# Optimization experiments

Measured on AMD Instinct MI355X. Metric: run time of the kernel, lower is better.

Reference implementation:

```python
import jax, jax.numpy as jnp
import numpy as np

N_NODES = 100000
N_EDGES = 600000
D_FEAT = 128
N_CLASSES = 64


def setup_inputs() -> dict:
    key = jax.random.key(0)
    k_h, k_src, k_dst, k_w = jax.random.split(key, 4)
    h = jax.random.normal(k_h, (N_NODES, D_FEAT), dtype=jnp.float32)
    src = jax.random.randint(k_src, (N_EDGES,), 0, N_NODES, dtype=jnp.int64)
    dst = jax.random.randint(k_dst, (N_EDGES,), 0, N_NODES, dtype=jnp.int64)
    # nn.Linear(2*D_FEAT, N_CLASSES): weight [out, in], bias [out]
    W = jax.random.normal(k_w, (N_CLASSES, 2 * D_FEAT), dtype=jnp.float32) * (1.0 / np.sqrt(2 * D_FEAT))
    b = jnp.zeros((N_CLASSES,), dtype=jnp.float32)
    return {"h": h, "src": src, "dst": dst, "W": W, "b": b}


def reference(h, src, dst, W, b):
    # score = Linear(concat([h[src], h[dst]], -1))
    # Split W to avoid materializing the [n_edges, 2*d] concat:
    # concat @ W.T == h[src] @ W[:, :d].T + h[dst] @ W[:, d:].T
    d = h.shape[1]
    Wu = W[:, :d]  # [out, d]
    Wv = W[:, d:]  # [out, d]
    score = (jnp.einsum('ed,cd->ec', h[src], Wu)
             + jnp.einsum('ed,cd->ec', h[dst], Wv)
             + b)
    return score  # [n_edges, out_classes]
```

## Files before the change

kernel.cpp:

```cpp
#include <hip/hip_runtime.h>

#define N_NODES   100000
#define N_EDGES   600000
#define D_FEAT    128
#define N_CLASSES 64

typedef short bf16x8 __attribute__((ext_vector_type(8)));
typedef float f32x4  __attribute__((ext_vector_type(4)));
typedef unsigned short u16x8 __attribute__((ext_vector_type(8)));

__device__ __forceinline__ unsigned short f2bf(float f) {
    unsigned int u = __float_as_uint(f);
    unsigned int r = (u + 0x7fffu + ((u >> 16) & 1u)) >> 16;
    return (unsigned short)r;
}
__device__ __forceinline__ float bf2f(unsigned short u) {
    return __uint_as_float((unsigned int)u << 16);
}

__global__ __launch_bounds__(256) void build_wcat(const float* __restrict__ W,
                                                  unsigned short* __restrict__ Wc) {
    int idx = blockIdx.x * 256 + threadIdx.x;
    int c = idx >> 7;
    int k = idx & 127;
    float v = (c < 64) ? W[c * 256 + k] : W[(c - 64) * 256 + 128 + k];
    Wc[c * 128 + k] = f2bf(v);
}

__global__ __launch_bounds__(256) void proj_mfma(const float* __restrict__ h,
                                                 const unsigned short* __restrict__ Wc,
                                                 const float* __restrict__ b,
                                                 unsigned short* __restrict__ P) {
    const int wave = (blockIdx.x * 256 + threadIdx.x) >> 6;
    const int lane = threadIdx.x & 63;
    const int n0   = wave * 16;
    if (n0 >= N_NODES) return;
    const int m    = lane & 15;
    const int quad = lane >> 4;

    bf16x8 hfrag[4];
    const float* hrow = h + (size_t)(n0 + m) * 128 + quad * 8;
#pragma unroll
    for (int ks = 0; ks < 4; ++ks) {
        f32x4 v0 = __builtin_nontemporal_load((const f32x4*)(hrow + ks * 32));
        f32x4 v1 = __builtin_nontemporal_load((const f32x4*)(hrow + ks * 32 + 4));
        bf16x8 a;
        a[0] = (short)f2bf(v0[0]); a[1] = (short)f2bf(v0[1]);
        a[2] = (short)f2bf(v0[2]); a[3] = (short)f2bf(v0[3]);
        a[4] = (short)f2bf(v1[0]); a[5] = (short)f2bf(v1[1]);
        a[6] = (short)f2bf(v1[2]); a[7] = (short)f2bf(v1[3]);
        hfrag[ks] = a;
    }

    f32x4 acc[8];
#pragma unroll
    for (int ct = 0; ct < 8; ++ct) acc[ct] = (f32x4){0.f, 0.f, 0.f, 0.f};

#pragma unroll
    for (int ct = 0; ct < 8; ++ct) {
        const unsigned short* wrow = Wc + (size_t)(ct * 16 + m) * 128 + quad * 8;
#pragma unroll
        for (int ks = 0; ks < 4; ++ks) {
            bf16x8 wfrag = *(const bf16x8*)(wrow + ks * 32);
            acc[ct] = __builtin_amdgcn_mfma_f32_16x16x32_bf16(wfrag, hfrag[ks], acc[ct], 0, 0, 0);
        }
    }

    const int node = n0 + m;
    unsigned short* prow = P + (size_t)node * 128;
#pragma unroll
    for (int ct = 0; ct < 8; ++ct) {
        const int cb = ct * 16 + quad * 4;
        float v[4];
        if (cb < 64) {
            f32x4 bb = *(const f32x4*)(b + cb);
#pragma unroll
            for (int r = 0; r < 4; ++r) v[r] = acc[ct][r] + bb[r];
        } else {
#pragma unroll
            for (int r = 0; r < 4; ++r) v[r] = acc[ct][r];
        }
        ushort4 pk;
        pk.x = f2bf(v[0]); pk.y = f2bf(v[1]);
        pk.z = f2bf(v[2]); pk.w = f2bf(v[3]);
        *(ushort4*)(prow + cb) = pk;
    }
}

__global__ __launch_bounds__(256) void edge_kernel(const int* __restrict__ src,
                                                   const int* __restrict__ dst,
                                                   const unsigned short* __restrict__ P,
                                                   float* __restrict__ out) {
    int g  = blockIdx.x * 256 + threadIdx.x;
    int e  = g >> 3;
    int c0 = (g & 7) << 3;
    int s = src[e];
    int d = dst[e];
    u16x8 us = *(const u16x8*)(P + (size_t)s * 128 + c0);
    u16x8 ud = *(const u16x8*)(P + (size_t)d * 128 + 64 + c0);
    f32x4 o0, o1;
    o0[0] = bf2f(us[0]) + bf2f(ud[0]);
    o0[1] = bf2f(us[1]) + bf2f(ud[1]);
    o0[2] = bf2f(us[2]) + bf2f(ud[2]);
    o0[3] = bf2f(us[3]) + bf2f(ud[3]);
    o1[0] = bf2f(us[4]) + bf2f(ud[4]);
    o1[1] = bf2f(us[5]) + bf2f(ud[5]);
    o1[2] = bf2f(us[6]) + bf2f(ud[6]);
    o1[3] = bf2f(us[7]) + bf2f(ud[7]);
    float* op = out + (size_t)e * 64 + c0;
    __builtin_nontemporal_store(o0, (f32x4*)op);
    __builtin_nontemporal_store(o1, (f32x4*)(op + 4));
}

__global__ __launch_bounds__(256) void direct_kernel(const float* __restrict__ h,
                                                     const int* __restrict__ src,
                                                     const int* __restrict__ dst,
                                                     const float* __restrict__ W,
                                                     const float* __restrict__ b,
                                                     float* __restrict__ out) {
    __shared__ float hcat[4][256];
    int t = threadIdx.x;
    int w = t >> 6, lane = t & 63;
    int e = blockIdx.x * 4 + w;
    bool valid = (e < N_EDGES);
    if (valid) {
        int s = src[e], d = dst[e];
        const float* p = (lane < 32) ? (h + (size_t)s * 128 + lane * 4)
                                     : (h + (size_t)d * 128 + (lane - 32) * 4);
        *(float4*)&hcat[w][lane * 4] = *(const float4*)p;
    }
    __syncthreads();
    if (!valid) return;
    int c = lane;
    float acc = 0.f;
    for (int k = 0; k < 256; k += 4) {
        float4 wv = *(const float4*)(W + c * 256 + k);
        acc += hcat[w][k] * wv.x + hcat[w][k + 1] * wv.y
             + hcat[w][k + 2] * wv.z + hcat[w][k + 3] * wv.w;
    }
    out[(size_t)e * 64 + c] = acc + b[c];
}

extern "C" void kernel_launch(void* const* d_in, const int* in_sizes, int n_in,
                              void* d_out, int out_size, void* d_ws, size_t ws_size,
                              hipStream_t stream) {
    const float* h   = (const float*)d_in[0];
    const int*   src = (const int*)d_in[1];
    const int*   dst = (const int*)d_in[2];
    const float* W   = (const float*)d_in[3];
    const float* b   = (const float*)d_in[4];
    float* out = (float*)d_out;

    const size_t wc_bytes = 128 * 128 * sizeof(unsigned short);
    const size_t p_bytes  = (size_t)N_NODES * 128 * sizeof(unsigned short);
    if (ws_size >= wc_bytes + p_bytes) {
        unsigned short* Wc = (unsigned short*)d_ws;
        unsigned short* P  = (unsigned short*)((char*)d_ws + wc_bytes);
        build_wcat<<<64, 256, 0, stream>>>(W, Wc);
        const int n_waves  = N_NODES / 16;
        const int n_blocks = (n_waves + 3) / 4;
        proj_mfma<<<n_blocks, 256, 0, stream>>>(h, Wc, b, P);
        edge_kernel<<<(N_EDGES * 8) / 256, 256, 0, stream>>>(src, dst, P, out);
    } else {
        direct_kernel<<<(N_EDGES + 3) / 4, 256, 0, stream>>>(h, src, dst, W, b, out);
    }
}
```

Measured before the change: 246.4 us.

## Fuse weight conversion into projection kernel via swizzled LDS and double edge work per thread

Removes the separate build_wcat launch. Each projection block now converts the fp32 weight matrix to bf16 itself and stores it in a 32KB XOR-swizzled shared-memory tile, so MFMA operand reads come from LDS without bank conflicts instead of from global memory. The edge kernel has each thread handle two edges half the edge range apart, which halves the grid and puts more independent gathers in flight. The trade-off is that every one of roughly 1563 blocks redoes the weight conversion and occupies 32KB of LDS, which can limit occupancy.

```diff
diff --git a/kernel.cpp b/kernel.cpp
--- a/kernel.cpp
+++ b/kernel.cpp
@@ -18,39 +18,54 @@
     return __uint_as_float((unsigned int)u << 16);
 }
 
-__global__ __launch_bounds__(256) void build_wcat(const float* __restrict__ W,
-                                                  unsigned short* __restrict__ Wc) {
-    int idx = blockIdx.x * 256 + threadIdx.x;
-    int c = idx >> 7;
-    int k = idx & 127;
-    float v = (c < 64) ? W[c * 256 + k] : W[(c - 64) * 256 + 128 + k];
-    Wc[c * 128 + k] = f2bf(v);
-}
-
 __global__ __launch_bounds__(256) void proj_mfma(const float* __restrict__ h,
-                                                 const unsigned short* __restrict__ Wc,
+                                                 const float* __restrict__ W,
                                                  const float* __restrict__ b,
                                                  unsigned short* __restrict__ P) {
+    __shared__ unsigned short WcS[128 * 128];
+
     const int wave = (blockIdx.x * 256 + threadIdx.x) >> 6;
     const int lane = threadIdx.x & 63;
     const int n0   = wave * 16;
-    if (n0 >= N_NODES) return;
+    const bool valid = (n0 < N_NODES);
     const int m    = lane & 15;
     const int quad = lane >> 4;
 
     bf16x8 hfrag[4];
-    const float* hrow = h + (size_t)(n0 + m) * 128 + quad * 8;
+    if (valid) {
+        const float* hrow = h + (size_t)(n0 + m) * 128 + quad * 8;
 #pragma unroll
-    for (int ks = 0; ks < 4; ++ks) {
-        f32x4 v0 = __builtin_nontemporal_load((const f32x4*)(hrow + ks * 32));
-        f32x4 v1 = __builtin_nontemporal_load((const f32x4*)(hrow + ks * 32 + 4));
-        bf16x8 a;
-        a[0] = (short)f2bf(v0[0]); a[1] = (short)f2bf(v0[1]);
-        a[2] = (short)f2bf(v0[2]); a[3] = (short)f2bf(v0[3]);
-        a[4] = (short)f2bf(v1[0]); a[5] = (short)f2bf(v1[1]);
-        a[6] = (short)f2bf(v1[2]); a[7] = (short)f2bf(v1[3]);
-        hfrag[ks] = a;
+        for (int ks = 0; ks < 4; ++ks) {
+            f32x4 v0 = __builtin_nontemporal_load((const f32x4*)(hrow + ks * 32));
+            f32x4 v1 = __builtin_nontemporal_load((const f32x4*)(hrow + ks * 32 + 4));
+            bf16x8 a;
+            a[0] = (short)f2bf(v0[0]); a[1] = (short)f2bf(v0[1]);
+            a[2] = (short)f2bf(v0[2]); a[3] = (short)f2bf(v0[3]);
+            a[4] = (short)f2bf(v1[0]); a[5] = (short)f2bf(v1[1]);
+            a[6] = (short)f2bf(v1[2]); a[7] = (short)f2bf(v1[3]);
+            hfrag[ks] = a;
+        }
     }
+
+    {
+        const int t = threadIdx.x;
+#pragma unroll
+        for (int i = 0; i < 16; ++i) {
+            int cc = i * 256 + t;
+            int c  = cc >> 5;
+            int kc = (cc & 31) << 2;
+            const float* wp = (c < 64) ? (W + c * 256 + kc)
+                                       : (W + (c - 64) * 256 + 128 + kc);
+            f32x4 v = *(const f32x4*)wp;
+            ushort4 pk;
+            pk.x = f2bf(v[0]); pk.y = f2bf(v[1]);
+            pk.z = f2bf(v[2]); pk.w = f2bf(v[3]);
+            int phys = (((kc >> 3) ^ (c & 15)) << 3) | (kc & 7);
+            *(ushort4*)(WcS + c * 128 + phys) = pk;
+        }
+    }
+    __syncthreads();
+    if (!valid) return;
 
     f32x4 acc[8];
 #pragma unroll
@@ -58,10 +73,10 @@
 
 #pragma unroll
     for (int ct = 0; ct < 8; ++ct) {
-        const unsigned short* wrow = Wc + (size_t)(ct * 16 + m) * 128 + quad * 8;
+        const unsigned short* wbase = WcS + (ct * 16 + m) * 128;
 #pragma unroll
         for (int ks = 0; ks < 4; ++ks) {
-            bf16x8 wfrag = *(const bf16x8*)(wrow + ks * 32);
+            bf16x8 wfrag = *(const bf16x8*)(wbase + (((ks * 4 + quad) ^ m) << 3));
             acc[ct] = __builtin_amdgcn_mfma_f32_16x16x32_bf16(wfrag, hfrag[ks], acc[ct], 0, 0, 0);
         }
     }
@@ -92,24 +107,30 @@
                                                    const unsigned short* __restrict__ P,
                                                    float* __restrict__ out) {
     int g  = blockIdx.x * 256 + threadIdx.x;
-    int e  = g >> 3;
+    int e0 = g >> 3;
     int c0 = (g & 7) << 3;
-    int s = src[e];
-    int d = dst[e];
-    u16x8 us = *(const u16x8*)(P + (size_t)s * 128 + c0);
-    u16x8 ud = *(const u16x8*)(P + (size_t)d * 128 + 64 + c0);
-    f32x4 o0, o1;
-    o0[0] = bf2f(us[0]) + bf2f(ud[0]);
-    o0[1] = bf2f(us[1]) + bf2f(ud[1]);
-    o0[2] = bf2f(us[2]) + bf2f(ud[2]);
-    o0[3] = bf2f(us[3]) + bf2f(ud[3]);
-    o1[0] = bf2f(us[4]) + bf2f(ud[4]);
-    o1[1] = bf2f(us[5]) + bf2f(ud[5]);
-    o1[2] = bf2f(us[6]) + bf2f(ud[6]);
-    o1[3] = bf2f(us[7]) + bf2f(ud[7]);
-    float* op = out + (size_t)e * 64 + c0;
-    __builtin_nontemporal_store(o0, (f32x4*)op);
-    __builtin_nontemporal_store(o1, (f32x4*)(op + 4));
+    int e1 = e0 + (N_EDGES / 2);
+    int s0 = src[e0], d0 = dst[e0];
+    int s1 = src[e1], d1 = dst[e1];
+    u16x8 us0 = *(const u16x8*)(P + (size_t)s0 * 128 + c0);
+    u16x8 ud0 = *(const u16x8*)(P + (size_t)d0 * 128 + 64 + c0);
+    u16x8 us1 = *(const u16x8*)(P + (size_t)s1 * 128 + c0);
+    u16x8 ud1 = *(const u16x8*)(P + (size_t)d1 * 128 + 64 + c0);
+
+    f32x4 a0, a1, b0, b1;
+#pragma unroll
+    for (int j = 0; j < 4; ++j) {
+        a0[j] = bf2f(us0[j])     + bf2f(ud0[j]);
+        a1[j] = bf2f(us0[j + 4]) + bf2f(ud0[j + 4]);
+        b0[j] = bf2f(us1[j])     + bf2f(ud1[j]);
+        b1[j] = bf2f(us1[j + 4]) + bf2f(ud1[j + 4]);
+    }
+    float* op0 = out + (size_t)e0 * 64 + c0;
+    float* op1 = out + (size_t)e1 * 64 + c0;
+    __builtin_nontemporal_store(a0, (f32x4*)op0);
+    __builtin_nontemporal_store(a1, (f32x4*)(op0 + 4));
+    __builtin_nontemporal_store(b0, (f32x4*)op1);
+    __builtin_nontemporal_store(b1, (f32x4*)(op1 + 4));
 }
 
 __global__ __launch_bounds__(256) void direct_kernel(const float* __restrict__ h,
@@ -151,16 +172,13 @@
     const float* b   = (const float*)d_in[4];
     float* out = (float*)d_out;
 
-    const size_t wc_bytes = 128 * 128 * sizeof(unsigned short);
-    const size_t p_bytes  = (size_t)N_NODES * 128 * sizeof(unsigned short);
-    if (ws_size >= wc_bytes + p_bytes) {
-        unsigned short* Wc = (unsigned short*)d_ws;
-        unsigned short* P  = (unsigned short*)((char*)d_ws + wc_bytes);
-        build_wcat<<<64, 256, 0, stream>>>(W, Wc);
+    const size_t p_bytes = (size_t)N_NODES * 128 * sizeof(unsigned short);
+    if (ws_size >= p_bytes) {
+        unsigned short* P = (unsigned short*)d_ws;
         const int n_waves  = N_NODES / 16;
         const int n_blocks = (n_waves + 3) / 4;
-        proj_mfma<<<n_blocks, 256, 0, stream>>>(h, Wc, b, P);
-        edge_kernel<<<(N_EDGES * 8) / 256, 256, 0, stream>>>(src, dst, P, out);
+        proj_mfma<<<n_blocks, 256, 0, stream>>>(h, W, b, P);
+        edge_kernel<<<(N_EDGES / 2 * 8) / 256, 256, 0, stream>>>(src, dst, P, out);
     } else {
         direct_kernel<<<(N_EDGES + 3) / 4, 256, 0, stream>>>(h, src, dst, W, b, out);
     }
```

Measured after the change: 234.4 us. 4.8% less time.
